# Performance work log

Hardware: AMD Instinct MI355X
Metric: run time of the kernel (lower is better)

Reference implementation:

```python
import jax, jax.numpy as jnp
import numpy as np

# All BatchNorms are in inference mode: folded to per-channel affine (g, b)
# where g = gamma/sqrt(running_var+eps), b = beta - running_mean*g.

def _conv(x, w, stride=1, pad=0, groups=1):
    return jax.lax.conv_general_dilated(
        x, w, (stride, stride), ((pad, pad), (pad, pad)),
        dimension_numbers=('NCHW', 'OIHW', 'NCHW'), feature_group_count=groups)

def _bn(x, g, b):
    return x * g[None, :, None, None] + b[None, :, None, None]

def _gn(x, g, b, eps=1e-5):
    # GroupNorm with 1 group: normalize over (C,H,W) per sample
    m = jnp.mean(x, axis=(1, 2, 3), keepdims=True)
    v = jnp.var(x, axis=(1, 2, 3), keepdims=True)
    return (x - m) * jax.lax.rsqrt(v + eps) * g[None, :, None, None] + b[None, :, None, None]

def _maxpool3(x):
    return jax.lax.reduce_window(x, -jnp.inf, jax.lax.max,
                                 (1, 1, 3, 3), (1, 1, 1, 1),
                                 ((0, 0), (0, 0), (1, 1), (1, 1)))


def reference(x, w_stem, g_stem, b_stem,
              w_cb1, g_cb1, b_cb1, w_cb2, g_cb2, b_cb2, w_cb3, g_cb3, b_cb3,
              w_cbres, g_cbres, b_cbres,
              w_lvc, g_lvc, b_lvc, codewords, cw_scale, g_enc, b_enc,
              w_fc, b_fc,
              gn1_g, gn1_b, w_dw, g_dw, b_dw, w_pw, g_pw, b_pw,
              gn2_g, gn2_b, w_fc1, bias_fc1, w_fc2, bias_fc2, ls1, ls2,
              w_cnv1, b_cnv1):
    relu = jax.nn.relu
    C = x.shape[1]
    # ---- stem: 7x7 conv + BN + ReLU + 3x3 maxpool (stride 1) ----
    x1 = _maxpool3(relu(_bn(_conv(x, w_stem, pad=3), g_stem, b_stem)))

    # ================= LVC branch =================
    # ConvBlock (res_conv=True, stride=1)
    t = relu(_bn(_conv(x1, w_cb1), g_cb1, b_cb1))           # 1x1 C->C/4
    t = relu(_bn(_conv(t, w_cb2, pad=1), g_cb2, b_cb2))     # 3x3 C/4->C/4
    t = _bn(_conv(t, w_cb3), g_cb3, b_cb3)                  # 1x1 C/4->C
    res = _bn(_conv(x1, w_cbres), g_cbres, b_cbres)         # 1x1 residual
    xc = relu(t + res)

    # LVC: 1x1 conv + BN + ReLU -> Encoding -> BN1d -> ReLU -> mean over codes
    z = relu(_bn(_conv(xc, w_lvc), g_lvc, b_lvc))
    b_, _, H, W = z.shape
    zf = z.reshape(b_, C, H * W).transpose(0, 2, 1)         # (b, N, C)
    # scaled L2: scale_k * ||x_n - c_k||^2, expanded (no (b,N,K,C) tensor)
    x2 = jnp.sum(zf * zf, axis=-1, keepdims=True)           # (b, N, 1)
    c2 = jnp.sum(codewords * codewords, axis=-1)            # (K,)
    dist = cw_scale * (x2 - 2.0 * jnp.einsum('bnc,kc->bnk', zf, codewords) + c2)
    A = jax.nn.softmax(dist, axis=2)                        # (b, N, K)
    # aggregate: sum_n A * (x - c) = A^T x - (sum_n A) * c
    en = jnp.einsum('bnk,bnc->bkc', A, zf) - A.sum(axis=1)[..., None] * codewords
    en = relu(en * g_enc[None, :, None] + b_enc[None, :, None])  # BN1d over codes
    en = en.mean(axis=1)                                    # (b, C)
    gam = jax.nn.sigmoid(en @ w_fc.T + b_fc)                # (b, C)
    x_lvc = relu(xc + xc * gam[:, :, None, None])

    # ================= LightMLP branch =================
    h = _gn(x1, gn1_g, gn1_b)
    h = jax.nn.silu(_bn(_conv(h, w_dw, groups=C), g_dw, b_dw))   # depthwise 1x1
    h = jax.nn.silu(_bn(_conv(h, w_pw), g_pw, b_pw))             # pointwise 1x1
    xm = x1 + ls1[None, :, None, None] * h
    h2 = _gn(xm, gn2_g, gn2_b)
    h2 = jax.nn.gelu(_conv(h2, w_fc1) + bias_fc1[None, :, None, None], approximate=False)
    h2 = _conv(h2, w_fc2) + bias_fc2[None, :, None, None]
    xm = xm + ls2[None, :, None, None] * h2

    # ---- fuse: concat + 1x1 conv ----
    out = _conv(jnp.concatenate([x_lvc, xm], axis=1), w_cnv1) + b_cnv1[None, :, None, None]
    return out


def setup_inputs() -> dict:
    B, C, H, W, K = 8, 256, 40, 40, 64
    c = C // 4
    HID = 4 * C
    key = jax.random.key(0)
    ks = iter(jax.random.split(key, 80))
    rn = lambda *s: jax.random.normal(next(ks), s, jnp.float32)
    un = lambda lo, hi, *s: jax.random.uniform(next(ks), s, jnp.float32, lo, hi)

    def aff(n):
        return un(0.8, 1.2, n), rn(n) * 0.1

    d = {}
    d['x'] = rn(B, C, H, W)
    d['w_stem'] = rn(C, C, 7, 7) * 0.01
    d['g_stem'], d['b_stem'] = aff(C)
    d['w_cb1'] = rn(c, C, 1, 1) * 0.05
    d['g_cb1'], d['b_cb1'] = aff(c)
    d['w_cb2'] = rn(c, c, 3, 3) * 0.05
    d['g_cb2'], d['b_cb2'] = aff(c)
    d['w_cb3'] = rn(C, c, 1, 1) * 0.05
    d['g_cb3'], d['b_cb3'] = aff(C)
    d['w_cbres'] = rn(C, C, 1, 1) * 0.05
    d['g_cbres'], d['b_cbres'] = aff(C)
    d['w_lvc'] = rn(C, C, 1, 1) * 0.05
    d['g_lvc'], d['b_lvc'] = aff(C)
    std = 1.0 / (K * C) ** 0.5
    d['codewords'] = un(-std, std, K, C)
    d['cw_scale'] = un(-1.0, 0.0, K)
    d['g_enc'], d['b_enc'] = aff(K)
    d['w_fc'] = rn(C, C) * 0.05
    d['b_fc'] = rn(C) * 0.1
    d['gn1_g'], d['gn1_b'] = aff(C)
    d['w_dw'] = rn(C, 1, 1, 1) * 0.5
    d['g_dw'], d['b_dw'] = aff(C)
    d['w_pw'] = rn(C, C, 1, 1) * 0.05
    d['g_pw'], d['b_pw'] = aff(C)
    d['gn2_g'], d['gn2_b'] = aff(C)
    d['w_fc1'] = rn(HID, C, 1, 1) * 0.05
    d['bias_fc1'] = rn(HID) * 0.02
    d['w_fc2'] = rn(C, HID, 1, 1) * 0.02
    d['bias_fc2'] = rn(C) * 0.02
    d['ls1'] = rn(C) * 0.1
    d['ls2'] = rn(C) * 0.1
    d['w_cnv1'] = rn(C, 2 * C, 1, 1) * 0.04
    d['b_cnv1'] = rn(C) * 0.02
    return d
```

## Files before the change

### kernel.cpp

```cpp
#include <hip/hip_runtime.h>
#include <hip/hip_bf16.h>
#include <math.h>

typedef unsigned short u16;
typedef u16 u16x4 __attribute__((ext_vector_type(4)));
typedef u16 u16x8 __attribute__((ext_vector_type(8)));
typedef short s16x8 __attribute__((ext_vector_type(8)));
typedef float f32x4 __attribute__((ext_vector_type(4)));

#define DEVI static __device__ __forceinline__

DEVI float bf2f(u16 u){ unsigned v=((unsigned)u)<<16; float f; __builtin_memcpy(&f,&v,4); return f; }
DEVI u16 f2bf(float f){ unsigned u; __builtin_memcpy(&u,&f,4); u=(u+0x7FFFu+((u>>16)&1u))>>16; return (u16)u; }

DEVI void gload16(const u16* g, u16* l){
  __builtin_amdgcn_global_load_lds(
      (const __attribute__((address_space(1))) void*)(unsigned long long)g,
      (__attribute__((address_space(3))) void*)(unsigned int)(unsigned long long)l,
      16, 0, 0);
}

constexpr size_t AL(size_t x){ return (x+511)&~(size_t)511; }
constexpr size_t sACT =8ull*1600*256*2;
constexpr size_t oXPAD=0;                constexpr size_t sXPAD=8ull*46*46*256*2;
constexpr size_t oT1P =AL(oXPAD+sXPAD);  constexpr size_t sT1P=8ull*42*42*64*2;
constexpr size_t oSTAT=AL(oT1P+sT1P);    constexpr size_t sSTAT=512;
constexpr size_t ZERO_BYTES=oSTAT+sSTAT;
constexpr size_t oWST =AL(ZERO_BYTES);   constexpr size_t sWST=6553600;
constexpr size_t oWCB2=AL(oWST+sWST);    constexpr size_t sWCB2=9*64*64*2;
constexpr size_t oWSM =AL(oWCB2+sWCB2);  constexpr size_t sWSM=901120ull*2;
constexpr size_t oC2  =AL(oWSM+sWSM);    constexpr size_t sC2=1024;
constexpr size_t oSTEM=AL(oC2+sC2);
constexpr size_t oX1  =AL(oSTEM+sACT);
constexpr size_t oT2  =AL(oX1+sACT);     constexpr size_t sT2=8ull*1600*64*2;
constexpr size_t oRRES=AL(oT2+sT2);
constexpr size_t oXC  =AL(oRRES+sACT);
constexpr size_t oZ   =AL(oXC+sACT);
constexpr size_t oZT  =AL(oZ+sACT);
constexpr size_t oX2  =AL(oZT+sACT);     constexpr size_t sX2=12800*4;
constexpr size_t oDOT =AL(oX2+sX2);      constexpr size_t sDOT=12800ull*64*4;
constexpr size_t oAS  =AL(oDOT+sDOT);    constexpr size_t sAS=64ull*12800*2;
constexpr size_t oASUM=AL(oAS+sAS);      constexpr size_t sASUM=512*4;
constexpr size_t oEN  =AL(oASUM+sASUM);  constexpr size_t sEN=8ull*64*256*4;
constexpr size_t oENM =AL(oEN+sEN);      constexpr size_t sENM=8*256*4;
constexpr size_t oGAM =AL(oENM+sENM);    constexpr size_t sGAM=8*256*4;
constexpr size_t oH2A =AL(oGAM+sGAM);    constexpr size_t sH2A=8ull*1600*1024*2;
constexpr size_t oFUSE=AL(oH2A+sH2A);    constexpr size_t sFUSE=8ull*1600*512*2;
constexpr size_t TOTAL_WS=oFUSE+sFUSE;
static_assert(TOTAL_WS < ((size_t)120<<20), "ws layout ~94MB");
constexpr size_t oPART =oRRES;             constexpr size_t sPART =7ull*12800*256*2;
constexpr size_t oPART2=oPART+sPART;       constexpr size_t sPART2=3ull*12800*64*2;
static_assert(oPART2+sPART2<=TOTAL_WS, "partials fit");

struct WCP { const float* s[9]; u16* d[9]; };
__global__ void wcast_plain(WCP p){
  int idx=blockIdx.x*256+threadIdx.x;
  int j,rel;
  if(idx<16384){j=0;rel=idx;}
  else if(idx<32768){j=1;rel=idx-16384;}
  else if(idx<98304){j=2;rel=idx-32768;}
  else if(idx<163840){j=3;rel=idx-98304;}
  else if(idx<229376){j=4;rel=idx-163840;}
  else if(idx<491520){j=5;rel=idx-229376;}
  else if(idx<753664){j=6;rel=idx-491520;}
  else if(idx<884736){j=7;rel=idx-753664;}
  else if(idx<901120){j=8;rel=idx-884736;}
  else return;
  p.d[j][rel]=f2bf(p.s[j][rel]);
}
__global__ void wcast_stem(const float* __restrict__ w, u16* __restrict__ o){
  __shared__ u16 sh[49*256];
  int co=blockIdx.x, ci=threadIdx.x;
  const float* src=w+(size_t)(co*256+ci)*49;
#pragma unroll 7
  for(int j=0;j<49;j++) sh[j*256+ci]=f2bf(src[j]);
  __syncthreads();
#pragma unroll 7
  for(int j=0;j<49;j++) o[((size_t)j*256+co)*256+ci]=sh[j*256+ci];
}
__global__ void wcast_cb2(const float* __restrict__ w, u16* __restrict__ o){
  int idx=blockIdx.x*256+threadIdx.x;
  if(idx>=9*4096) return;
  int ci=idx&63; int t=idx>>6; int co=t&63; int dhw=t>>6;
  o[idx]=f2bf(w[(co*64+ci)*9+dhw]);
}
__global__ void c2k(const float* __restrict__ cw, float* __restrict__ c2){
  int k=threadIdx.x; if(k>=64) return;
  float s=0.f;
  for(int i=0;i<256;i++){ float v=cw[k*256+i]; s+=v*v; }
  c2[k]=s;
}

__global__ void x_to_xpad(const float* __restrict__ x, u16* __restrict__ xpad){
  __shared__ u16 sh[40*257];
  int h=blockIdx.x, z=blockIdx.y;
  const float* xb=x+(size_t)z*409600+h*40;
  for(int e=threadIdx.x;e<10240;e+=256){ int c=e/40, w=e-40*(e/40); sh[w*257+c]=f2bf(xb[c*1600+w]); }
  __syncthreads();
  u16* op=xpad+((size_t)(z*46+h+3)*46+3)*256;
  for(int e=threadIdx.x;e<10240;e+=256){ int w=e>>8, c=e&255; op[w*256+c]=sh[w*257+c]; }
}

template<int COT,int COTOT,int PXT,int CIN,int PW,int KS,int NW,int TPS,int TTOT,int NSLICE,int XSWZ>
__global__ __launch_bounds__(NW*64) void conv_lds(
    const u16* __restrict__ Xp, const u16* __restrict__ Wt, u16* __restrict__ part){
  constexpr int WPN=PXT/64;
  constexpr int WGR=COT/16;
  constexpr int AGR=PXT/16;
  constexpr int IW=WGR/NW;
  constexpr int IA=AGR/NW;
  constexpr int CST=CIN/32;
  constexpr int CSH=(CST==8)?3:1;

  __shared__ __align__(16) u16 sW[2][COT*32];
  __shared__ __align__(16) u16 sA[2][PXT*32];

  const int wv=threadIdx.x>>6, ln=threadIdx.x&63, lr=ln&15, kg=ln>>4;
  const int wr=wv/WPN, wc=wv%WPN;
  int co0,px0,slice;
  if constexpr(XSWZ){
    int lin=blockIdx.x; int xcd=lin&7, rest=lin>>3;
    int combo=rest/13, pxin=rest%13;
    int pxt=xcd*13+pxin;
    if(pxt>=100) return;
    slice=combo>>1; co0=(combo&1)*COT; px0=pxt*PXT;
  } else {
    co0=blockIdx.x*COT; px0=blockIdx.y*PXT; slice=blockIdx.z;
  }
  const int tb=slice*TPS;
  const int te=(slice==NSLICE-1)?TTOT:(tb+TPS);
  const int nst=(te-tb)<<CSH;

  int wbase[IW], abase[IA];
#pragma unroll
  for(int q=0;q<IW;q++){
    int g=wv*IW+q;
    wbase[q]=(co0+g*16+lr)*CIN+kg*8;
  }
#pragma unroll
  for(int q=0;q<IA;q++){
    int g=wv*IA+q;
    int p=px0+g*16+lr;
    int z=p/1600, rem=p-z*1600;
    int h=rem/40, w=rem-h*40;
    abase[q]=((z*PW+h)*PW+w)*CIN+kg*8;
  }

  f32x4 acc[4][4];
#pragma unroll
  for(int i=0;i<4;i++)
#pragma unroll
    for(int j=0;j<4;j++) acc[i][j]=f32x4{0.f,0.f,0.f,0.f};

  auto stage=[&](int buf,int s){
    int ti=tb+(s>>CSH);
    int c0=(s&(CST-1))<<5;
    int dh=ti/KS, dw=ti-dh*KS;
    const u16* wsrc=Wt+(size_t)ti*COTOT*CIN+c0;
    int aoff=(dh*PW+dw)*CIN+c0;
#pragma unroll
    for(int q=0;q<IW;q++) gload16(wsrc+wbase[q], &sW[buf][(wv*IW+q)*512]);
#pragma unroll
    for(int q=0;q<IA;q++) gload16(Xp+abase[q]+aoff, &sA[buf][(wv*IA+q)*512]);
  };
  auto compute=[&](int buf){
    s16x8 av[4], bv[4];
#pragma unroll
    for(int i=0;i<4;i++) av[i]=*(const s16x8*)(&sW[buf][(wr*4+i)*512+ln*8]);
#pragma unroll
    for(int j=0;j<4;j++) bv[j]=*(const s16x8*)(&sA[buf][(wc*4+j)*512+ln*8]);
#pragma unroll
    for(int i=0;i<4;i++)
#pragma unroll
      for(int j=0;j<4;j++)
        acc[i][j]=__builtin_amdgcn_mfma_f32_16x16x32_bf16(av[i],bv[j],acc[i][j],0,0,0);
  };

  stage(0,0);
  for(int s=0;s<nst;s++){
    __syncthreads();
    if(s+1<nst) stage((s+1)&1, s+1);
    compute(s&1);
  }

  u16* pb=part+(size_t)slice*12800*COTOT;
#pragma unroll
  for(int i=0;i<4;i++){
    int co=co0+wr*64+i*16+kg*4;
#pragma unroll
    for(int j=0;j<4;j++){
      int px=px0+wc*64+j*16+lr;
      u16x4 o;
#pragma unroll
      for(int q=0;q<4;q++) o[q]=f2bf(acc[i][j][q]);
      *(u16x4*)(pb+(size_t)px*COTOT+co)=o;
    }
  }
}

template<int MT8,int NS>
__global__ void ep_red(const u16* __restrict__ part, const float* __restrict__ g,
    const float* __restrict__ b, u16* __restrict__ out){
  int t=blockIdx.x*256+threadIdx.x;
  int c=(t%MT8)*8; int gp=t/MT8;
  size_t base=(size_t)gp*(MT8*8)+c;
  constexpr size_t SS=(size_t)12800*MT8*8;
  float v[8];
#pragma unroll
  for(int q=0;q<8;q++) v[q]=0.f;
#pragma unroll
  for(int s=0;s<NS;s++){
    u16x8 a=*(const u16x8*)(part+s*SS+base);
#pragma unroll
    for(int q=0;q<8;q++) v[q]+=bf2f(a[q]);
  }
  u16x8 o;
#pragma unroll
  for(int q=0;q<8;q++) o[q]=f2bf(fmaxf(v[q]*g[c+q]+b[c+q],0.f));
  *(u16x8*)(out+base)=o;
}

__global__ void maxpool3(const u16* __restrict__ in, u16* __restrict__ out){
  int t=blockIdx.x*256+threadIdx.x;
  int c8=(t&31)*8; int gp=t>>5;
  int n=gp%1600; int z=gp/1600; int h=n/40, w=n%40;
  float mx[8];
#pragma unroll
  for(int q=0;q<8;q++) mx[q]=-1e30f;
  for(int dh=-1;dh<=1;dh++){ int hh=h+dh; if((unsigned)hh>=40u) continue;
    for(int dw=-1;dw<=1;dw++){ int ww=w+dw; if((unsigned)ww>=40u) continue;
      u16x8 v=*(const u16x8*)(in+((size_t)z*1600+hh*40+ww)*256+c8);
#pragma unroll
      for(int q=0;q<8;q++) mx[q]=fmaxf(mx[q],bf2f(v[q]));
    }}
  u16x8 o;
#pragma unroll
  for(int q=0;q<8;q++) o[q]=f2bf(mx[q]);
  *(u16x8*)(out+((size_t)z*1600+n)*256+c8)=o;
}

struct GP {
  const u16* A; long long Asz; int lda;
  const u16* Bp; long long Bsz; int ldb;
  int Kd;
  const float *e0,*e1,*e2,*e3;
  const u16* r0;
  u16* ob; float* of; u16* ob2;
  int ldo;
};

template<int MF,int NF,int EPI>
__global__ __launch_bounds__(256) void gemm_nt(GP p){
  const int wv=threadIdx.x>>6, ln=threadIdx.x&63, lr=ln&15, kg=ln>>4;
  int z=blockIdx.z, kc=0;
  if constexpr(EPI==11){ kc=z%5; z=z/5; }
  const int m0=blockIdx.x*(MF*64)+wv*(MF*16);
  const int n0=blockIdx.y*(NF*16);
  const u16* A=p.A+(size_t)z*p.Asz+kc*320;
  const u16* Bb=p.Bp+(size_t)z*p.Bsz+kc*320;
  const u16* ar[MF]; const u16* br[NF];
#pragma unroll
  for(int i=0;i<MF;i++) ar[i]=A+(size_t)(m0+i*16+lr)*p.lda+kg*8;
#pragma unroll
  for(int j=0;j<NF;j++) br[j]=Bb+(size_t)(n0+j*16+lr)*p.ldb+kg*8;
  f32x4 acc[MF][NF];
#pragma unroll
  for(int i=0;i<MF;i++)
#pragma unroll
    for(int j=0;j<NF;j++) acc[i][j]=f32x4{0.f,0.f,0.f,0.f};
  int k=0;
  for(;k+64<=p.Kd;k+=64){
    s16x8 av0[MF], bv0[NF], av1[MF], bv1[NF];
#pragma unroll
    for(int i=0;i<MF;i++){ av0[i]=*(const s16x8*)(ar[i]+k); av1[i]=*(const s16x8*)(ar[i]+k+32); }
#pragma unroll
    for(int j=0;j<NF;j++){ bv0[j]=*(const s16x8*)(br[j]+k); bv1[j]=*(const s16x8*)(br[j]+k+32); }
#pragma unroll
    for(int i=0;i<MF;i++)
#pragma unroll
      for(int j=0;j<NF;j++)
        acc[i][j]=__builtin_amdgcn_mfma_f32_16x16x32_bf16(av0[i],bv0[j],acc[i][j],0,0,0);
#pragma unroll
    for(int i=0;i<MF;i++)
#pragma unroll
      for(int j=0;j<NF;j++)
        acc[i][j]=__builtin_amdgcn_mfma_f32_16x16x32_bf16(av1[i],bv1[j],acc[i][j],0,0,0);
  }
  for(;k<p.Kd;k+=32){
    s16x8 av[MF], bv[NF];
#pragma unroll
    for(int i=0;i<MF;i++) av[i]=*(const s16x8*)(ar[i]+k);
#pragma unroll
    for(int j=0;j<NF;j++) bv[j]=*(const s16x8*)(br[j]+k);
#pragma unroll
    for(int i=0;i<MF;i++)
#pragma unroll
      for(int j=0;j<NF;j++)
        acc[i][j]=__builtin_amdgcn_mfma_f32_16x16x32_bf16(av[i],bv[j],acc[i][j],0,0,0);
  }
#pragma unroll
  for(int i=0;i<MF;i++){
    const int mb=m0+i*16+kg*4;
#pragma unroll
    for(int j=0;j<NF;j++){
      const int n=n0+j*16+lr;
      f32x4 v=acc[i][j];
      if constexpr(EPI==1){
        int h=n/40, w=n%40;
        u16x4 o;
#pragma unroll
        for(int q=0;q<4;q++) o[q]=f2bf(fmaxf(v[q]*p.e0[mb+q]+p.e1[mb+q],0.f));
        *(u16x4*)(p.ob+((size_t)z*1764+(h+1)*42+(w+1))*64+mb)=o;
      } else if constexpr(EPI==2){
        u16x4 o;
#pragma unroll
        for(int q=0;q<4;q++) o[q]=f2bf(v[q]*p.e0[mb+q]+p.e1[mb+q]);
        *(u16x4*)(p.ob+((size_t)z*1600+n)*256+mb)=o;
      } else if constexpr(EPI==3){
        u16x4 rv=*(const u16x4*)(p.r0+((size_t)z*1600+n)*256+mb);
        u16x4 o;
#pragma unroll
        for(int q=0;q<4;q++) o[q]=f2bf(fmaxf(v[q]*p.e0[mb+q]+p.e1[mb+q]+bf2f(rv[q]),0.f));
        *(u16x4*)(p.ob+((size_t)z*1600+n)*256+mb)=o;
      } else if constexpr(EPI==4){
        u16x4 o;
#pragma unroll
        for(int q=0;q<4;q++) o[q]=f2bf(fmaxf(v[q]*p.e0[mb+q]+p.e1[mb+q],0.f));
        *(u16x4*)(p.ob+((size_t)z*1600+n)*256+mb)=o;
#pragma unroll
        for(int q=0;q<4;q++) p.ob2[((size_t)z*256+mb+q)*1600+n]=o[q];
      } else if constexpr(EPI==5){
#pragma unroll
        for(int q=0;q<4;q++) p.of[(size_t)(mb+q)*64+n]=v[q];
      } else if constexpr(EPI==7){
        u16x4 o;
#pragma unroll
        for(int q=0;q<4;q++){ float t=v[q]+p.e0[mb+q]; t=0.5f*t*(1.f+erff(t*0.70710678f)); o[q]=f2bf(t); }
        *(u16x4*)(p.ob+((size_t)z*1600+n)*p.ldo+mb)=o;
      } else if constexpr(EPI==8){
        u16x4 rv=*(const u16x4*)(p.r0+((size_t)z*1600+n)*256+mb);
        u16x4 o;
#pragma unroll
        for(int q=0;q<4;q++){ float t=v[q]+p.e0[mb+q]; o[q]=f2bf(bf2f(rv[q])+p.e1[mb+q]*t); }
        *(u16x4*)(p.ob+((size_t)z*1600+n)*512+mb)=o;
      } else if constexpr(EPI==9){
        u16x4 rv=*(const u16x4*)(p.r0+((size_t)z*1600+n)*256+mb);
        u16x4 o;
#pragma unroll
        for(int q=0;q<4;q++){ float t=v[q]*p.e0[mb+q]+p.e1[mb+q]; float s=t/(1.f+expf(-t));
          o[q]=f2bf(bf2f(rv[q])+p.e2[mb+q]*s); }
        *(u16x4*)(p.ob+((size_t)z*1600+n)*256+mb)=o;
      } else if constexpr(EPI==10){
#pragma unroll
        for(int q=0;q<4;q++) p.of[((size_t)z*256+mb+q)*1600+n]=v[q]+p.e0[mb+q];
      } else if constexpr(EPI==11){
#pragma unroll
        for(int q=0;q<4;q++) atomicAdd(&p.of[((size_t)z*64+mb+q)*256+n],v[q]);
      }
    }
  }
}

__global__ void rowsq(const u16* __restrict__ zb, float* __restrict__ x2){
  int wv=threadIdx.x>>6, ln=threadIdx.x&63;
  int gp=blockIdx.x*4+wv;
  u16x4 v=*(const u16x4*)(zb+(size_t)gp*256+ln*4);
  float s=0.f;
#pragma unroll
  for(int q=0;q<4;q++){ float f=bf2f(v[q]); s+=f*f; }
  for(int d=32;d;d>>=1) s+=__shfl_xor(s,d);
  if(ln==0) x2[gp]=s;
}

__global__ void softmax_k(const float* __restrict__ dot, const float* __restrict__ x2,
    const float* __restrict__ c2, const float* __restrict__ cws, u16* __restrict__ As){
  int wv=threadIdx.x>>6, ln=threadIdx.x&63;
  int base=blockIdx.x*64+wv*16;
  float sc=cws[ln], cc=c2[ln];
  for(int it=0;it<16;it++){
    int gp=base+it;
    float d=sc*(x2[gp]-2.f*dot[(size_t)gp*64+ln]+cc);
    float m=d;
    for(int o=32;o;o>>=1) m=fmaxf(m,__shfl_xor(m,o));
    float e=expf(d-m);
    float s=e;
    for(int o=32;o;o>>=1) s+=__shfl_xor(s,o);
    As[(size_t)ln*12800+gp]=f2bf(e/s);
  }
}

__global__ void asum_k(const u16* __restrict__ As, float* __restrict__ Asum){
  int wv=threadIdx.x>>6, ln=threadIdx.x&63;
  int id=blockIdx.x*4+wv;
  int b=id>>6, k=id&63;
  const u16* r=As+(size_t)k*12800+b*1600;
  float s=0.f;
  for(int i=ln;i<1600;i+=64) s+=bf2f(r[i]);
  for(int o=32;o;o>>=1) s+=__shfl_xor(s,o);
  if(ln==0) Asum[id]=s;
}

__global__ void enmean_ep(const float* __restrict__ enraw, const float* __restrict__ Asum,
    const float* __restrict__ cw, const float* __restrict__ g, const float* __restrict__ b,
    float* __restrict__ enm){
  int bz=blockIdx.x, c=threadIdx.x;
  float s=0.f;
  for(int k=0;k<64;k++){
    float t=(enraw[((size_t)bz*64+k)*256+c]-Asum[bz*64+k]*cw[k*256+c])*g[k]+b[k];
    s+=fmaxf(t,0.f);
  }
  enm[bz*256+c]=s*(1.f/64.f);
}

__global__ void fc_sig(const float* __restrict__ enm, const float* __restrict__ wfc,
    const float* __restrict__ bfc, float* __restrict__ gam){
  __shared__ float sh[256];
  int b=blockIdx.x, co=threadIdx.x;
  sh[co]=enm[b*256+co];
  __syncthreads();
  float s=bfc[co];
  for(int i=0;i<256;i++) s+=sh[i]*wfc[co*256+i];
  gam[b*256+co]=1.f/(1.f+expf(-s));
}

__global__ void ew_xlvc(const u16* __restrict__ xc, const float* __restrict__ gam, u16* __restrict__ fb){
  int t=blockIdx.x*256+threadIdx.x;
  int c=(t&31)*8; int gp=t>>5; int z=gp/1600;
  u16x8 v=*(const u16x8*)(xc+(size_t)gp*256+c);
  u16x8 o;
#pragma unroll
  for(int q=0;q<8;q++){ float ga=1.f+gam[z*256+c+q]; o[q]=f2bf(fmaxf(bf2f(v[q])*ga,0.f)); }
  *(u16x8*)(fb+(size_t)gp*512+c)=o;
}

__global__ void gn_stats(const u16* __restrict__ x, float* __restrict__ st){
  int z=blockIdx.y;
  const u16* pz=x+(size_t)z*409600;
  float s=0.f, ss=0.f;
  for(int i=blockIdx.x*256+threadIdx.x;i<51200;i+=gridDim.x*256){
    u16x8 v=*(const u16x8*)(pz+(size_t)i*8);
#pragma unroll
    for(int q=0;q<8;q++){ float f=bf2f(v[q]); s+=f; ss+=f*f; }
  }
  for(int o=32;o;o>>=1){ s+=__shfl_xor(s,o); ss+=__shfl_xor(ss,o); }
  __shared__ float sh[8];
  int wv=threadIdx.x>>6, ln=threadIdx.x&63;
  if(ln==0){ sh[wv]=s; sh[4+wv]=ss; }
  __syncthreads();
  if(threadIdx.x==0){
    atomicAdd(&st[z*2],  sh[0]+sh[1]+sh[2]+sh[3]);
    atomicAdd(&st[z*2+1],sh[4]+sh[5]+sh[6]+sh[7]);
  }
}

__global__ void ew_hdw(const u16* __restrict__ x1, const float* __restrict__ st,
    const float* __restrict__ g1, const float* __restrict__ b1,
    const float* __restrict__ wdw, const float* __restrict__ gdw, const float* __restrict__ bdw,
    u16* __restrict__ out){
  int t=blockIdx.x*256+threadIdx.x;
  int c=(t&31)*8; int gp=t>>5; int z=gp/1600;
  float mean=st[z*2]*(1.f/409600.f);
  float var=st[z*2+1]*(1.f/409600.f)-mean*mean;
  float rs=rsqrtf(var+1e-5f);
  u16x8 v=*(const u16x8*)(x1+(size_t)gp*256+c);
  u16x8 o;
#pragma unroll
  for(int q=0;q<8;q++){
    int cc=c+q;
    float t0=(bf2f(v[q])-mean)*rs*g1[cc]+b1[cc];
    t0=t0*wdw[cc]*gdw[cc]+bdw[cc];
    o[q]=f2bf(t0/(1.f+expf(-t0)));
  }
  *(u16x8*)(out+(size_t)gp*256+c)=o;
}

__global__ void ew_gn2(const u16* __restrict__ xm, const float* __restrict__ st,
    const float* __restrict__ g2, const float* __restrict__ b2, u16* __restrict__ out){
  int t=blockIdx.x*256+threadIdx.x;
  int c=(t&31)*8; int gp=t>>5; int z=gp/1600;
  float mean=st[z*2]*(1.f/409600.f);
  float var=st[z*2+1]*(1.f/409600.f)-mean*mean;
  float rs=rsqrtf(var+1e-5f);
  u16x8 v=*(const u16x8*)(xm+(size_t)gp*256+c);
  u16x8 o;
#pragma unroll
  for(int q=0;q<8;q++){ int cc=c+q; o[q]=f2bf((bf2f(v[q])-mean)*rs*g2[cc]+b2[cc]); }
  *(u16x8*)(out+(size_t)gp*256+c)=o;
}

extern "C" void kernel_launch(void* const* d_in, const int* in_sizes, int n_in,
                              void* d_out, int out_size, void* d_ws, size_t ws_size,
                              hipStream_t stream){
  const float* X    =(const float*)d_in[0];
  const float* Wstem=(const float*)d_in[1];
  const float* Gstem=(const float*)d_in[2];
  const float* Bstem=(const float*)d_in[3];
  const float* Wcb1 =(const float*)d_in[4];
  const float* Gcb1 =(const float*)d_in[5];
  const float* Bcb1 =(const float*)d_in[6];
  const float* Wcb2 =(const float*)d_in[7];
  const float* Gcb2 =(const float*)d_in[8];
  const float* Bcb2 =(const float*)d_in[9];
  const float* Wcb3 =(const float*)d_in[10];
  const float* Gcb3 =(const float*)d_in[11];
  const float* Bcb3 =(const float*)d_in[12];
  const float* Wres =(const float*)d_in[13];
  const float* Gres =(const float*)d_in[14];
  const float* Bres =(const float*)d_in[15];
  const float* Wlvc =(const float*)d_in[16];
  const float* Glvc =(const float*)d_in[17];
  const float* Blvc =(const float*)d_in[18];
  const float* CW   =(const float*)d_in[19];
  const float* CWS  =(const float*)d_in[20];
  const float* Genc =(const float*)d_in[21];
  const float* Benc =(const float*)d_in[22];
  const float* Wfc  =(const float*)d_in[23];
  const float* Bfc  =(const float*)d_in[24];
  const float* GN1g =(const float*)d_in[25];
  const float* GN1b =(const float*)d_in[26];
  const float* Wdw  =(const float*)d_in[27];
  const float* Gdw  =(const float*)d_in[28];
  const float* Bdw  =(const float*)d_in[29];
  const float* Wpw  =(const float*)d_in[30];
  const float* Gpw  =(const float*)d_in[31];
  const float* Bpw  =(const float*)d_in[32];
  const float* GN2g =(const float*)d_in[33];
  const float* GN2b =(const float*)d_in[34];
  const float* Wfc1 =(const float*)d_in[35];
  const float* Bfc1 =(const float*)d_in[36];
  const float* Wfc2 =(const float*)d_in[37];
  const float* Bfc2 =(const float*)d_in[38];
  const float* LS1  =(const float*)d_in[39];
  const float* LS2  =(const float*)d_in[40];
  const float* Wcnv =(const float*)d_in[41];
  const float* Bcnv =(const float*)d_in[42];
  char* ws=(char*)d_ws;
  if(ws_size < TOTAL_WS) return;

  u16* xpad=(u16*)(ws+oXPAD);
  u16* t1p =(u16*)(ws+oT1P);
  float* stats=(float*)(ws+oSTAT);
  u16* wst =(u16*)(ws+oWST);
  u16* wcb2t=(u16*)(ws+oWCB2);
  u16* wsm =(u16*)(ws+oWSM);
  float* c2b=(float*)(ws+oC2);
  u16* act =(u16*)(ws+oSTEM);
  u16* x1  =(u16*)(ws+oX1);
  u16* t2  =(u16*)(ws+oT2);
  u16* rres=(u16*)(ws+oRRES);
  u16* xc  =(u16*)(ws+oXC);
  u16* zb  =(u16*)(ws+oZ);
  u16* zt  =(u16*)(ws+oZT);
  float* x2b=(float*)(ws+oX2);
  float* dotb=(float*)(ws+oDOT);
  u16* As  =(u16*)(ws+oAS);
  float* Asum=(float*)(ws+oASUM);
  float* enraw=(float*)(ws+oEN);
  float* enm=(float*)(ws+oENM);
  float* gam=(float*)(ws+oGAM);
  u16* h2a =(u16*)(ws+oH2A);
  u16* fb  =(u16*)(ws+oFUSE);
  u16* xm  =(u16*)(ws+oXPAD);
  u16* xmgn=(u16*)(ws+oWST);
  u16* hdw =(u16*)(ws+oRRES);
  u16* accP =(u16*)(ws+oPART);
  u16* accP2=(u16*)(ws+oPART2);
  u16* wcb1=wsm+0;      u16* wcb3=wsm+16384;  u16* wresb=wsm+32768; u16* wlvcb=wsm+98304;
  u16* wpwb=wsm+163840; u16* wfc1b=wsm+229376;u16* wfc2b=wsm+491520;u16* wcnvb=wsm+753664;
  u16* cwb=wsm+884736;

  hipMemsetAsync(d_ws,0,ZERO_BYTES,stream);
  { WCP p;
    p.s[0]=Wcb1;p.d[0]=wcb1;  p.s[1]=Wcb3;p.d[1]=wcb3;  p.s[2]=Wres;p.d[2]=wresb;
    p.s[3]=Wlvc;p.d[3]=wlvcb; p.s[4]=Wpw;p.d[4]=wpwb;   p.s[5]=Wfc1;p.d[5]=wfc1b;
    p.s[6]=Wfc2;p.d[6]=wfc2b; p.s[7]=Wcnv;p.d[7]=wcnvb; p.s[8]=CW;p.d[8]=cwb;
    wcast_plain<<<3520,256,0,stream>>>(p); }
  wcast_stem<<<256,256,0,stream>>>(Wstem,wst);
  wcast_cb2<<<144,256,0,stream>>>(Wcb2,wcb2t);
  c2k<<<1,64,0,stream>>>(CW,c2b);
  x_to_xpad<<<dim3(40,8),256,0,stream>>>(X,xpad);

  conv_lds<128,256,128,256,46,7,4,7,49,7,1><<<1456,256,0,stream>>>(xpad,wst,accP);
  ep_red<32,7><<<1600,256,0,stream>>>(accP,Gstem,Bstem,act);
  maxpool3<<<1600,256,0,stream>>>(act,x1);

  { GP p{}; p.A=wcb1;p.Asz=0;p.lda=256; p.Bp=x1;p.Bsz=1600*256;p.ldb=256; p.Kd=256;
    p.e0=Gcb1;p.e1=Bcb1; p.ob=t1p;
    gemm_nt<1,5,1><<<dim3(1,20,8),256,0,stream>>>(p); }
  conv_lds<64,64,128,64,42,3,2,3,9,3,0><<<dim3(1,100,3),128,0,stream>>>(t1p,wcb2t,accP2);
  ep_red<8,3><<<400,256,0,stream>>>(accP2,Gcb2,Bcb2,t2);
  { GP p{}; p.A=wresb;p.Asz=0;p.lda=256; p.Bp=x1;p.Bsz=1600*256;p.ldb=256; p.Kd=256;
    p.e0=Gres;p.e1=Bres; p.ob=rres;
    gemm_nt<2,5,2><<<dim3(2,20,8),256,0,stream>>>(p); }
  { GP p{}; p.A=wcb3;p.Asz=0;p.lda=64; p.Bp=t2;p.Bsz=1600*64;p.ldb=64; p.Kd=64;
    p.e0=Gcb3;p.e1=Bcb3; p.r0=rres; p.ob=xc;
    gemm_nt<2,5,3><<<dim3(2,20,8),256,0,stream>>>(p); }
  { GP p{}; p.A=wlvcb;p.Asz=0;p.lda=256; p.Bp=xc;p.Bsz=1600*256;p.ldb=256; p.Kd=256;
    p.e0=Glvc;p.e1=Blvc; p.ob=zb; p.ob2=zt;
    gemm_nt<2,5,4><<<dim3(2,20,8),256,0,stream>>>(p); }
  rowsq<<<3200,256,0,stream>>>(zb,x2b);
  { GP p{}; p.A=zb;p.Asz=0;p.lda=256; p.Bp=cwb;p.Bsz=0;p.ldb=256; p.Kd=256; p.of=dotb;
    gemm_nt<2,4,5><<<dim3(100,1,1),256,0,stream>>>(p); }
  softmax_k<<<200,256,0,stream>>>(dotb,x2b,c2b,CWS,As);
  asum_k<<<128,256,0,stream>>>(As,Asum);
  hipMemsetAsync(enraw,0,sEN,stream);
  { GP p{}; p.A=As;p.Asz=1600;p.lda=12800; p.Bp=zt;p.Bsz=256*1600;p.ldb=1600; p.Kd=320;
    p.of=enraw;
    gemm_nt<1,4,11><<<dim3(1,4,40),256,0,stream>>>(p); }
  enmean_ep<<<8,256,0,stream>>>(enraw,Asum,CW,Genc,Benc,enm);
  fc_sig<<<8,256,0,stream>>>(enm,Wfc,Bfc,gam);
  ew_xlvc<<<1600,256,0,stream>>>(xc,gam,fb);

  gn_stats<<<dim3(25,8),256,0,stream>>>(x1,stats);
  ew_hdw<<<1600,256,0,stream>>>(x1,stats,GN1g,GN1b,Wdw,Gdw,Bdw,hdw);
  { GP p{}; p.A=wpwb;p.Asz=0;p.lda=256; p.Bp=hdw;p.Bsz=1600*256;p.ldb=256; p.Kd=256;
    p.e0=Gpw;p.e1=Bpw;p.e2=LS1; p.r0=x1; p.ob=xm;
    gemm_nt<2,5,9><<<dim3(2,20,8),256,0,stream>>>(p); }
  gn_stats<<<dim3(25,8),256,0,stream>>>(xm,stats+16);
  ew_gn2<<<1600,256,0,stream>>>(xm,stats+16,GN2g,GN2b,xmgn);
  { GP p{}; p.A=wfc1b;p.Asz=0;p.lda=256; p.Bp=xmgn;p.Bsz=1600*256;p.ldb=256; p.Kd=256;
    p.e0=Bfc1; p.ob=h2a; p.ldo=1024;
    gemm_nt<2,5,7><<<dim3(8,20,8),256,0,stream>>>(p); }
  { GP p{}; p.A=wfc2b;p.Asz=0;p.lda=1024; p.Bp=h2a;p.Bsz=1600*1024;p.ldb=1024; p.Kd=1024;
    p.e0=Bfc2;p.e1=LS2; p.r0=xm; p.ob=fb+256;
    gemm_nt<2,5,8><<<dim3(2,20,8),256,0,stream>>>(p); }
  { GP p{}; p.A=wcnvb;p.Asz=0;p.lda=512; p.Bp=fb;p.Bsz=1600*512;p.ldb=512; p.Kd=512;
    p.e0=Bcnv; p.of=(float*)d_out;
    gemm_nt<2,5,10><<<dim3(2,20,8),256,0,stream>>>(p); }
}
```

Measured before the change: 709.5 us.

## Swizzle conv LDS layout, fuse tiny kernels, nontemporal partial stores, simplify gemm K loop

The conv_lds kernel now remaps which lane loads which 16-byte chunk and XOR-swizzles the LDS read offsets. The aim is to cut bank conflicts on the MFMA fragment reads. Its partial-sum stores become nontemporal. The codeword-norm kernel is folded into an extra block of the weight-cast kernel, and the encoding-mean and FC-sigmoid kernels are merged into one, removing launches. The gemm_nt K loop drops its two-step unroll, which may reduce register pressure but gives up some load/MFMA overlap.

```diff
diff --git a/kernel.cpp b/kernel.cpp
--- a/kernel.cpp
+++ b/kernel.cpp
@@ -52,8 +52,13 @@
 constexpr size_t oPART2=oPART+sPART;       constexpr size_t sPART2=3ull*12800*64*2;
 static_assert(oPART2+sPART2<=TOTAL_WS, "partials fit");
 
-struct WCP { const float* s[9]; u16* d[9]; };
+struct WCP { const float* s[9]; u16* d[9]; const float* cw; float* c2; };
 __global__ void wcast_plain(WCP p){
+  if(blockIdx.x==3520){
+    int k=threadIdx.x;
+    if(k<64){ float s=0.f; for(int i=0;i<256;i++){ float v=p.cw[k*256+i]; s+=v*v; } p.c2[k]=s; }
+    return;
+  }
   int idx=blockIdx.x*256+threadIdx.x;
   int j,rel;
   if(idx<16384){j=0;rel=idx;}
@@ -84,12 +89,6 @@
   int ci=idx&63; int t=idx>>6; int co=t&63; int dhw=t>>6;
   o[idx]=f2bf(w[(co*64+ci)*9+dhw]);
 }
-__global__ void c2k(const float* __restrict__ cw, float* __restrict__ c2){
-  int k=threadIdx.x; if(k>=64) return;
-  float s=0.f;
-  for(int i=0;i<256;i++){ float v=cw[k*256+i]; s+=v*v; }
-  c2[k]=s;
-}
 
 __global__ void x_to_xpad(const float* __restrict__ x, u16* __restrict__ xpad){
   __shared__ u16 sh[40*257];
@@ -117,6 +116,8 @@
 
   const int wv=threadIdx.x>>6, ln=threadIdx.x&63, lr=ln&15, kg=ln>>4;
   const int wr=wv/WPN, wc=wv%WPN;
+  const int colq=((ln&3)^((ln>>3)&3))*8;
+  const int fofs=(lr*4+(kg^((lr>>1)&3)))*8;
   int co0,px0,slice;
   if constexpr(XSWZ){
     int lin=blockIdx.x; int xcd=lin&7, rest=lin>>3;
@@ -135,15 +136,15 @@
 #pragma unroll
   for(int q=0;q<IW;q++){
     int g=wv*IW+q;
-    wbase[q]=(co0+g*16+lr)*CIN+kg*8;
+    wbase[q]=(co0+g*16+(ln>>2))*CIN+colq;
   }
 #pragma unroll
   for(int q=0;q<IA;q++){
     int g=wv*IA+q;
-    int p=px0+g*16+lr;
+    int p=px0+g*16+(ln>>2);
     int z=p/1600, rem=p-z*1600;
     int h=rem/40, w=rem-h*40;
-    abase[q]=((z*PW+h)*PW+w)*CIN+kg*8;
+    abase[q]=((z*PW+h)*PW+w)*CIN+colq;
   }
 
   f32x4 acc[4][4];
@@ -166,9 +167,9 @@
   auto compute=[&](int buf){
     s16x8 av[4], bv[4];
 #pragma unroll
-    for(int i=0;i<4;i++) av[i]=*(const s16x8*)(&sW[buf][(wr*4+i)*512+ln*8]);
-#pragma unroll
-    for(int j=0;j<4;j++) bv[j]=*(const s16x8*)(&sA[buf][(wc*4+j)*512+ln*8]);
+    for(int i=0;i<4;i++) av[i]=*(const s16x8*)(&sW[buf][(wr*4+i)*512+fofs]);
+#pragma unroll
+    for(int j=0;j<4;j++) bv[j]=*(const s16x8*)(&sA[buf][(wc*4+j)*512+fofs]);
 #pragma unroll
     for(int i=0;i<4;i++)
 #pragma unroll
@@ -193,7 +194,8 @@
       u16x4 o;
 #pragma unroll
       for(int q=0;q<4;q++) o[q]=f2bf(acc[i][j][q]);
-      *(u16x4*)(pb+(size_t)px*COTOT+co)=o;
+      unsigned long long pk; __builtin_memcpy(&pk,&o,8);
+      __builtin_nontemporal_store(pk,(unsigned long long*)(pb+(size_t)px*COTOT+co));
     }
   }
 }
@@ -268,25 +270,7 @@
   for(int i=0;i<MF;i++)
 #pragma unroll
     for(int j=0;j<NF;j++) acc[i][j]=f32x4{0.f,0.f,0.f,0.f};
-  int k=0;
-  for(;k+64<=p.Kd;k+=64){
-    s16x8 av0[MF], bv0[NF], av1[MF], bv1[NF];
-#pragma unroll
-    for(int i=0;i<MF;i++){ av0[i]=*(const s16x8*)(ar[i]+k); av1[i]=*(const s16x8*)(ar[i]+k+32); }
-#pragma unroll
-    for(int j=0;j<NF;j++){ bv0[j]=*(const s16x8*)(br[j]+k); bv1[j]=*(const s16x8*)(br[j]+k+32); }
-#pragma unroll
-    for(int i=0;i<MF;i++)
-#pragma unroll
-      for(int j=0;j<NF;j++)
-        acc[i][j]=__builtin_amdgcn_mfma_f32_16x16x32_bf16(av0[i],bv0[j],acc[i][j],0,0,0);
-#pragma unroll
-    for(int i=0;i<MF;i++)
-#pragma unroll
-      for(int j=0;j<NF;j++)
-        acc[i][j]=__builtin_amdgcn_mfma_f32_16x16x32_bf16(av1[i],bv1[j],acc[i][j],0,0,0);
-  }
-  for(;k<p.Kd;k+=32){
+  for(int k=0;k<p.Kd;k+=32){
     s16x8 av[MF], bv[NF];
 #pragma unroll
     for(int i=0;i<MF;i++) av[i]=*(const s16x8*)(ar[i]+k);
@@ -400,27 +384,21 @@
   if(ln==0) Asum[id]=s;
 }
 
-__global__ void enmean_ep(const float* __restrict__ enraw, const float* __restrict__ Asum,
+__global__ void enc_tail(const float* __restrict__ enraw, const float* __restrict__ Asum,
     const float* __restrict__ cw, const float* __restrict__ g, const float* __restrict__ b,
-    float* __restrict__ enm){
+    const float* __restrict__ wfc, const float* __restrict__ bfc, float* __restrict__ gam){
+  __shared__ float sh[256];
   int bz=blockIdx.x, c=threadIdx.x;
   float s=0.f;
   for(int k=0;k<64;k++){
     float t=(enraw[((size_t)bz*64+k)*256+c]-Asum[bz*64+k]*cw[k*256+c])*g[k]+b[k];
     s+=fmaxf(t,0.f);
   }
-  enm[bz*256+c]=s*(1.f/64.f);
-}
-
-__global__ void fc_sig(const float* __restrict__ enm, const float* __restrict__ wfc,
-    const float* __restrict__ bfc, float* __restrict__ gam){
-  __shared__ float sh[256];
-  int b=blockIdx.x, co=threadIdx.x;
-  sh[co]=enm[b*256+co];
+  sh[c]=s*(1.f/64.f);
   __syncthreads();
-  float s=bfc[co];
-  for(int i=0;i<256;i++) s+=sh[i]*wfc[co*256+i];
-  gam[b*256+co]=1.f/(1.f+expf(-s));
+  float acc=bfc[c];
+  for(int i=0;i<256;i++) acc+=sh[i]*wfc[c*256+i];
+  gam[bz*256+c]=1.f/(1.f+expf(-acc));
 }
 
 __global__ void ew_xlvc(const u16* __restrict__ xc, const float* __restrict__ gam, u16* __restrict__ fb){
@@ -556,7 +534,6 @@
   u16* As  =(u16*)(ws+oAS);
   float* Asum=(float*)(ws+oASUM);
   float* enraw=(float*)(ws+oEN);
-  float* enm=(float*)(ws+oENM);
   float* gam=(float*)(ws+oGAM);
   u16* h2a =(u16*)(ws+oH2A);
   u16* fb  =(u16*)(ws+oFUSE);
@@ -574,10 +551,10 @@
     p.s[0]=Wcb1;p.d[0]=wcb1;  p.s[1]=Wcb3;p.d[1]=wcb3;  p.s[2]=Wres;p.d[2]=wresb;
     p.s[3]=Wlvc;p.d[3]=wlvcb; p.s[4]=Wpw;p.d[4]=wpwb;   p.s[5]=Wfc1;p.d[5]=wfc1b;
     p.s[6]=Wfc2;p.d[6]=wfc2b; p.s[7]=Wcnv;p.d[7]=wcnvb; p.s[8]=CW;p.d[8]=cwb;
-    wcast_plain<<<3520,256,0,stream>>>(p); }
+    p.cw=CW; p.c2=c2b;
+    wcast_plain<<<3521,256,0,stream>>>(p); }
   wcast_stem<<<256,256,0,stream>>>(Wstem,wst);
   wcast_cb2<<<144,256,0,stream>>>(Wcb2,wcb2t);
-  c2k<<<1,64,0,stream>>>(CW,c2b);
   x_to_xpad<<<dim3(40,8),256,0,stream>>>(X,xpad);
 
   conv_lds<128,256,128,256,46,7,4,7,49,7,1><<<1456,256,0,stream>>>(xpad,wst,accP);
@@ -607,8 +584,7 @@
   { GP p{}; p.A=As;p.Asz=1600;p.lda=12800; p.Bp=zt;p.Bsz=256*1600;p.ldb=1600; p.Kd=320;
     p.of=enraw;
     gemm_nt<1,4,11><<<dim3(1,4,40),256,0,stream>>>(p); }
-  enmean_ep<<<8,256,0,stream>>>(enraw,Asum,CW,Genc,Benc,enm);
-  fc_sig<<<8,256,0,stream>>>(enm,Wfc,Bfc,gam);
+  enc_tail<<<8,256,0,stream>>>(enraw,Asum,CW,Genc,Benc,Wfc,Bfc,gam);
   ew_xlvc<<<1600,256,0,stream>>>(xc,gam,fb);
 
   gn_stats<<<dim3(25,8),256,0,stream>>>(x1,stats);
```

New measurement: 641.6 us. 9.6% less time.
